# Kernel tuning notes

Measured on AMD Instinct MI355X. Metric: run time of the kernel, lower is better.

The kernel has to match this reference:

```python
import jax, jax.numpy as jnp
import numpy as np

# Layered-DAG regularization of the dynamic active_path graph.
H, N, BATCH, D, R = 6, 16, 32, 512, 64   # hop levels, nodes/level, batch, dim, low-rank
M = (H - 1) * N                           # nodes with weights (levels 1..H-1)
ETA_W = 0.015
LAM_C, LAM_R = 0.65, 0.35
THETA0 = 0.5
SPEC_MIN, SPEC_MAX = 0.3, 4.0
BETA1, BETA2, EPS = 0.9, 0.999, 1e-8
W_MAX = float(np.sqrt(D) * 2.0)
DW_CLIP = 5.0


def _spectral_norm(A1, B1):
    # largest singular value of W = A1 @ B1.T via power iteration using only low-rank products
    d = A1.shape[0]
    def body(_, u):
        w = A1 @ (B1.T @ (B1 @ (A1.T @ u)))  # (W W^T) u
        return w / (jnp.linalg.norm(w) + 1e-12)
    u0 = jnp.ones((d,), A1.dtype) / jnp.sqrt(jnp.asarray(d, A1.dtype))
    u = jax.lax.fori_loop(0, 20, body, u0)
    return jnp.linalg.norm(B1 @ (A1.T @ u))


def _update_node(A1, B1, mA, vA, mB, vB, Vin, T_local):
    # dual-signal (contrastive + retrograde) weight update, Adam step t=1, is_positive=True
    W = A1 @ B1.T                       # (D, D)
    Vw = Vin @ W.T                      # (BATCH, D) pre-activation (record.V_weighted)
    Vout = jnp.tanh(Vw)                 # record.V_out (tanh primitive)
    fprime = 1.0 - Vout ** 2            # primitive_derivative for tanh
    goodness = (Vout ** 2).sum(-1).mean()
    theta = THETA0 * ((Vin ** 2).sum(-1).mean() + 1e-9)   # goodness_scale_input=True
    delta = goodness - theta
    Vout_grad = (Vout * fprime * delta).mean(0)
    Vin_mean = Vin.mean(0)
    dW_c = jnp.outer(Vout_grad, Vin_mean)
    dW_r = jnp.outer(T_local.mean(0) * fprime.mean(0), Vin_mean)
    dW = LAM_C * dW_c + LAM_R * dW_r
    gnorm = jnp.linalg.norm(dW)
    dW = dW * jnp.where(gnorm > DW_CLIP, DW_CLIP / (gnorm + 1e-12), 1.0)
    gA = dW @ B1
    gB = dW.T @ A1
    mA_n = BETA1 * mA + (1 - BETA1) * gA
    vA_n = BETA2 * vA + (1 - BETA2) * gA ** 2
    A_new = A1 - ETA_W * (mA_n / (1 - BETA1)) / (jnp.sqrt(vA_n / (1 - BETA2)) + EPS)
    mB_n = BETA1 * mB + (1 - BETA1) * gB
    vB_n = BETA2 * vB + (1 - BETA2) * gB ** 2
    B_new = B1 - ETA_W * (mB_n / (1 - BETA1)) / (jnp.sqrt(vB_n / (1 - BETA2)) + EPS)
    return jnp.clip(A_new, -W_MAX, W_MAX), jnp.clip(B_new, -W_MAX, W_MAX)


def _forward(Y_hat, Y_star, V_edges, A, Bw, m_A, v_A, m_B, v_B):
    T_v = (Y_star - Y_hat) / jnp.sqrt(jnp.asarray(D, Y_hat.dtype))
    mse = jnp.mean((Y_star - Y_hat) ** 2)

    # proportional blame: per-edge mean-over-batch L2 norm of the contribution
    norms = jnp.linalg.norm(V_edges, axis=-1).mean(-1)           # (H-1, Ndst, Nsrc)
    w_blame = norms / (norms.sum(-1, keepdims=True) + 1e-9)

    spec = jax.vmap(jax.vmap(_spectral_norm))(A, Bw)             # (H-1, N)
    scale = jax.lax.stop_gradient(jnp.clip(spec, SPEC_MIN, SPEC_MAX))  # torch.tensor() detaches

    # retrograde flow in reverse topological (hop) order; output node = (level H-1, node 0)
    T_top = jnp.zeros((N, BATCH, D), Y_hat.dtype).at[0].set(T_v)

    def step(T_curr, xs):
        w_h, s_h = xs                                            # (Ndst,Nsrc), (Ndst,)
        tnorm = jnp.linalg.norm(T_curr, axis=-1).mean(-1)        # (Ndst,)
        edge_t = s_h[:, None] * w_h * tnorm[:, None]             # ||T_upstream|| per edge
        T_prev = jnp.einsum('j,ji,jbd->ibd', s_h, w_h, T_curr)   # blame-weighted scatter
        return T_prev, (T_prev, edge_t)

    _, (Ts, edge_t) = jax.lax.scan(step, T_top, (w_blame[::-1], scale[::-1]))
    T_all = jnp.concatenate([Ts[::-1], T_top[None]], axis=0)     # (H, N, BATCH, D), by level
    edge_tensions = edge_t[::-1]                                 # (H-1, Ndst, Nsrc)

    V_in = V_edges.sum(axis=2)                                   # inbox sum -> (H-1, N, BATCH, D)
    T_upd = T_all[1:]                                            # tensions at non-input nodes

    sh = (M, D, R)
    A_new, B_new = jax.vmap(_update_node)(
        A.reshape(sh), Bw.reshape(sh), m_A.reshape(sh), v_A.reshape(sh),
        m_B.reshape(sh), v_B.reshape(sh),
        V_in.reshape(M, BATCH, D), T_upd.reshape(M, BATCH, D))
    return (mse, edge_tensions,
            A_new.reshape(H - 1, N, D, R), B_new.reshape(H - 1, N, D, R), T_all)


def setup_inputs():
    key = jax.random.key(0)
    k = jax.random.split(key, 7)
    sd = 1.0 / np.sqrt(D)
    return {
        "Y_hat": jax.random.normal(k[0], (BATCH, D), jnp.float32),
        "Y_star": jax.random.normal(k[1], (BATCH, D), jnp.float32),
        "V_edges": jax.random.normal(k[2], (H - 1, N, N, BATCH, D), jnp.float32),
        "A": jax.random.normal(k[3], (H - 1, N, D, R), jnp.float32) * sd,
        "Bw": jax.random.normal(k[4], (H - 1, N, D, R), jnp.float32) * sd,
        "m_A": jnp.zeros((H - 1, N, D, R), jnp.float32),
        "v_A": jax.random.uniform(k[5], (H - 1, N, D, R), jnp.float32) * 1e-4,
        "m_B": jnp.zeros((H - 1, N, D, R), jnp.float32),
        "v_B": jax.random.uniform(k[6], (H - 1, N, D, R), jnp.float32) * 1e-4,
    }


def reference(Y_hat, Y_star, V_edges, A, Bw, m_A, v_A, m_B, v_B):
    return _forward(Y_hat, Y_star, V_edges, A, Bw, m_A, v_A, m_B, v_B)
```

## Files before the change

### kernel.cpp

```cpp
#include <hip/hip_runtime.h>
#include <math.h>

#define DEV static __device__ __forceinline__

constexpr int NB    = 16;
constexpr int BATCH = 32;
constexpr int DDIM  = 512;
constexpr int RK    = 64;
constexpr int LAY   = 5;
constexpr int MM    = 80;
constexpr int TLS   = NB * BATCH * DDIM;

constexpr float ETA_W   = 0.015f;
constexpr float LAM_C   = 0.65f, LAM_R = 0.35f;
constexpr float THETA0  = 0.5f;
constexpr float SPEC_MIN = 0.3f, SPEC_MAX = 4.0f;
constexpr float DW_CLIP = 5.0f;
constexpr float W_MAX   = 45.254833995939045f;
constexpr float RSQ_D   = 0.044194173824159216f;

constexpr int OUT_MSE  = 0;
constexpr int OUT_EDGE = 1;
constexpr int OUT_A    = 1281;
constexpr int OUT_B    = OUT_A + MM * DDIM * RK;
constexpr int OUT_T    = OUT_B + MM * DDIM * RK;

constexpr int SCR_GP   = 1284;
constexpr int SCR_VIN  = SCR_GP + 2621440;

constexpr int WS_NORMB  = 0;
constexpr int WS_TVN    = 40960;
constexpr int WS_COEF   = 40992;
constexpr int WS_C      = 43520;
constexpr int WS_SCALE  = 44800;
constexpr int WS_Y0P    = 44880;
constexpr int WS_VM     = 65360;
constexpr int WS_P      = 106320;
constexpr int WS_Q      = 111440;
constexpr int WS_GC     = 116560;

DEV float wave_reduce(float v) {
  #pragma unroll
  for (int o = 32; o > 0; o >>= 1) v += __shfl_down(v, o, 64);
  return v;
}

DEV float block_reduce_512(float v, float* sred) {
  v = wave_reduce(v);
  __syncthreads();
  if ((threadIdx.x & 63) == 0) sred[threadIdx.x >> 6] = v;
  __syncthreads();
  float s = 0.f;
  #pragma unroll
  for (int k = 0; k < 8; ++k) s += sred[k];
  return s;
}

DEV float bcast_lane(float v, int lane) {
  return __int_as_float(__builtin_amdgcn_readlane(__float_as_int(v), lane));
}

__global__ void kmse(const float* __restrict__ yh, const float* __restrict__ ys,
                     float* __restrict__ out) {
  __shared__ float sred[16];
  int t = threadIdx.x;
  float s = 0.f;
  for (int i = t; i < 4096; i += 1024) {
    float4 a = ((const float4*)yh)[i], b = ((const float4*)ys)[i];
    float d0 = b.x - a.x, d1 = b.y - a.y, d2 = b.z - a.z, d3 = b.w - a.w;
    s += d0*d0 + d1*d1 + d2*d2 + d3*d3;
  }
  s = wave_reduce(s);
  if ((t & 63) == 0) sred[t >> 6] = s;
  __syncthreads();
  if (t == 0) {
    float tot = 0.f;
    #pragma unroll
    for (int k = 0; k < 16; ++k) tot += sred[k];
    out[OUT_MSE] = tot * (1.f / 16384.f);
  }
}

__global__ void k_tvnorm(const float* __restrict__ yh, const float* __restrict__ ys,
                         float* __restrict__ ws) {
  __shared__ float sred[4];
  int b = blockIdx.x, t = threadIdx.x;
  float2 a = ((const float2*)(yh + (size_t)b * 512))[t];
  float2 c = ((const float2*)(ys + (size_t)b * 512))[t];
  float d0 = c.x - a.x, d1 = c.y - a.y;
  float s = d0*d0 + d1*d1;
  s = wave_reduce(s);
  if ((t & 63) == 0) sred[t >> 6] = s;
  __syncthreads();
  if (t == 0)
    ws[WS_TVN + b] = sqrtf(sred[0] + sred[1] + sred[2] + sred[3]) * RSQ_D;
}

__global__ void k_vin_norm(const float* __restrict__ V, float* __restrict__ out,
                           float* __restrict__ ws) {
  __shared__ float sbuf[16][256];
  int bid = blockIdx.x;
  int b = bid & 31, j = (bid >> 5) & 15, hh = bid >> 9;
  const float* base = V + (size_t)(((hh*16 + j)*16)*32 + b) * 512;
  int t = threadIdx.x;
  float ax = 0.f, ay = 0.f;
  #pragma unroll
  for (int i = 0; i < 16; ++i) {
    float2 vv = ((const float2*)(base + (size_t)i * 16384))[t];
    sbuf[i][t] = vv.x*vv.x + vv.y*vv.y;
    ax += vv.x; ay += vv.y;
  }
  float2 o; o.x = ax; o.y = ay;
  ((float2*)(out + SCR_VIN + (size_t)((hh*16 + j)*32 + b) * 512))[t] = o;
  __syncthreads();
  int w = t >> 6, lane = t & 63;
  #pragma unroll
  for (int k = 0; k < 4; ++k) {
    int i = w * 4 + k;
    float s = sbuf[i][lane] + sbuf[i][lane+64] + sbuf[i][lane+128] + sbuf[i][lane+192];
    s = wave_reduce(s);
    if (lane == 0)
      ws[WS_NORMB + (size_t)((hh*16 + j)*16 + i) * 32 + b] = sqrtf(s);
  }
}

__global__ void k_gram(const float* __restrict__ Aw, const float* __restrict__ Bww,
                       float* __restrict__ out, float* __restrict__ ws) {
  __shared__ float tile[128 * 64];
  __shared__ float y0s[4][64];
  int bid = blockIdx.x;
  int slice = bid & 3, side = (bid >> 2) & 1, m = bid >> 3;
  const float* src = (side ? Bww : Aw) + (size_t)m * 32768 + slice * 8192;
  int t = threadIdx.x;
  #pragma unroll
  for (int k = 0; k < 8; ++k)
    ((float4*)tile)[t + k * 256] = ((const float4*)src)[t + k * 256];
  __syncthreads();
  {
    int r = t & 63, q = t >> 6;
    float s = 0.f;
    #pragma unroll 8
    for (int dd = q * 32; dd < q * 32 + 32; ++dd) s += tile[dd * 64 + r];
    y0s[q][r] = s;
  }
  __syncthreads();
  if (side == 0 && t < 64)
    ws[WS_Y0P + (m * 4 + slice) * 64 + t] = y0s[0][t] + y0s[1][t] + y0s[2][t] + y0s[3][t];
  float acc[4][4];
  #pragma unroll
  for (int i = 0; i < 4; ++i)
    #pragma unroll
    for (int k = 0; k < 4; ++k) acc[i][k] = 0.f;
  int r1 = (t >> 4) * 4, r2 = (t & 15) * 4;
  #pragma unroll 4
  for (int dd = 0; dd < 128; ++dd) {
    float4 a1 = *(const float4*)&tile[dd * 64 + r1];
    float4 a2 = *(const float4*)&tile[dd * 64 + r2];
    float av[4] = {a1.x, a1.y, a1.z, a1.w};
    float bv[4] = {a2.x, a2.y, a2.z, a2.w};
    #pragma unroll
    for (int i = 0; i < 4; ++i)
      #pragma unroll
      for (int k = 0; k < 4; ++k) acc[i][k] += av[i] * bv[k];
  }
  float* outp = out + SCR_GP + (size_t)((m * 2 + side) * 4 + slice) * 4096;
  #pragma unroll
  for (int i = 0; i < 4; ++i) {
    float4 v; v.x = acc[i][0]; v.y = acc[i][1]; v.z = acc[i][2]; v.w = acc[i][3];
    *(float4*)&outp[(r1 + i) * 64 + r2] = v;
  }
}

__global__ __launch_bounds__(64, 1) void k_power(const float* __restrict__ out,
                                                 float* __restrict__ ws) {
  int m = blockIdx.x;
  int r = threadIdx.x;
  const float* gp = out + SCR_GP + (size_t)(m * 2 + 0) * 16384;
  const float* hp = out + SCR_GP + (size_t)(m * 2 + 1) * 16384;
  float Gc[64], Hc[64];
  #pragma unroll
  for (int c4 = 0; c4 < 16; ++c4) {
    const float* gb = gp + r * 64 + c4 * 4;
    float4 g0 = *(const float4*)(gb);
    float4 g1 = *(const float4*)(gb + 4096);
    float4 g2 = *(const float4*)(gb + 8192);
    float4 g3 = *(const float4*)(gb + 12288);
    Gc[c4*4+0] = g0.x+g1.x+g2.x+g3.x;
    Gc[c4*4+1] = g0.y+g1.y+g2.y+g3.y;
    Gc[c4*4+2] = g0.z+g1.z+g2.z+g3.z;
    Gc[c4*4+3] = g0.w+g1.w+g2.w+g3.w;
    const float* hb = hp + r * 64 + c4 * 4;
    float4 h0 = *(const float4*)(hb);
    float4 h1 = *(const float4*)(hb + 4096);
    float4 h2 = *(const float4*)(hb + 8192);
    float4 h3 = *(const float4*)(hb + 12288);
    Hc[c4*4+0] = h0.x+h1.x+h2.x+h3.x;
    Hc[c4*4+1] = h0.y+h1.y+h2.y+h3.y;
    Hc[c4*4+2] = h0.z+h1.z+h2.z+h3.z;
    Hc[c4*4+3] = h0.w+h1.w+h2.w+h3.w;
  }
  float y = (ws[WS_Y0P + (m*4+0)*64 + r] + ws[WS_Y0P + (m*4+1)*64 + r] +
             ws[WS_Y0P + (m*4+2)*64 + r] + ws[WS_Y0P + (m*4+3)*64 + r]) * RSQ_D;
  for (int it = 0; it < 20; ++it) {
    float z0 = 0.f, z1 = 0.f, z2 = 0.f, z3 = 0.f;
    #pragma unroll
    for (int c = 0; c < 16; ++c) {
      z0 = fmaf(Hc[c],      bcast_lane(y, c),      z0);
      z1 = fmaf(Hc[c + 16], bcast_lane(y, c + 16), z1);
      z2 = fmaf(Hc[c + 32], bcast_lane(y, c + 32), z2);
      z3 = fmaf(Hc[c + 48], bcast_lane(y, c + 48), z3);
    }
    float z = (z0 + z1) + (z2 + z3);
    float t0 = 0.f, t1 = 0.f, t2 = 0.f, t3 = 0.f;
    #pragma unroll
    for (int c = 0; c < 16; ++c) {
      t0 = fmaf(Gc[c],      bcast_lane(z, c),      t0);
      t1 = fmaf(Gc[c + 16], bcast_lane(z, c + 16), t1);
      t2 = fmaf(Gc[c + 32], bcast_lane(z, c + 32), t2);
      t3 = fmaf(Gc[c + 48], bcast_lane(z, c + 48), t3);
    }
    float tt = (t0 + t1) + (t2 + t3);
    float zt = z * tt;
    #pragma unroll
    for (int o = 32; o > 0; o >>= 1) zt += __shfl_xor(zt, o, 64);
    y = tt / (sqrtf(zt) + 1e-12f);
  }
  float z0 = 0.f, z1 = 0.f, z2 = 0.f, z3 = 0.f;
  #pragma unroll
  for (int c = 0; c < 16; ++c) {
    z0 = fmaf(Hc[c],      bcast_lane(y, c),      z0);
    z1 = fmaf(Hc[c + 16], bcast_lane(y, c + 16), z1);
    z2 = fmaf(Hc[c + 32], bcast_lane(y, c + 32), z2);
    z3 = fmaf(Hc[c + 48], bcast_lane(y, c + 48), z3);
  }
  float z = (z0 + z1) + (z2 + z3);
  float yz = y * z;
  #pragma unroll
  for (int o = 32; o > 0; o >>= 1) yz += __shfl_xor(yz, o, 64);
  if (r == 0)
    ws[WS_SCALE + m] = fminf(fmaxf(sqrtf(yz), SPEC_MIN), SPEC_MAX);
}

__global__ void k_coef(float* __restrict__ ws) {
  int hh = blockIdx.x, t = threadIdx.x;
  int j = t >> 4;
  const float* nb = ws + WS_NORMB + (size_t)(hh * 256 + t) * 32;
  float n = 0.f;
  #pragma unroll 8
  for (int b = 0; b < 32; ++b) n += nb[b];
  n *= (1.f / 32.f);
  float s = n;
  s += __shfl_xor(s, 1, 64);
  s += __shfl_xor(s, 2, 64);
  s += __shfl_xor(s, 4, 64);
  s += __shfl_xor(s, 8, 64);
  ws[WS_C + hh * 256 + t] = ws[WS_SCALE + hh * 16 + j] * n / (s + 1e-9f);
}

__global__ void k_chain(float* __restrict__ ws, float* __restrict__ out) {
  __shared__ float C[5 * 256];
  __shared__ float coef[6 * 16];
  int t = threadIdx.x;
  #pragma unroll
  for (int k = 0; k < 5; ++k) C[k * 256 + t] = ws[WS_C + k * 256 + t];
  if (t < 16) coef[5 * 16 + t] = (t == 0) ? 1.f : 0.f;
  __syncthreads();
  if (t < 16) {
    for (int h = 4; h >= 0; --h) {
      float s = 0.f;
      #pragma unroll
      for (int j = 0; j < 16; ++j) s += C[h * 256 + j * 16 + t] * coef[(h + 1) * 16 + j];
      coef[h * 16 + t] = s;
    }
  }
  __syncthreads();
  float tvs = 0.f;
  #pragma unroll
  for (int b = 0; b < 32; ++b) tvs += ws[WS_TVN + b];
  float tvmean = tvs * (1.f / 32.f);
  #pragma unroll
  for (int h = 0; h < 5; ++h)
    out[OUT_EDGE + h * 256 + t] = C[h * 256 + t] * coef[(h + 1) * 16 + (t >> 4)] * tvmean;
  if (t < 96) ws[WS_COEF + t] = coef[t];
}

__global__ void k_twrite(const float* __restrict__ yh, const float* __restrict__ ys,
                         const float* __restrict__ ws, float* __restrict__ out) {
  int gid = blockIdx.x * 256 + threadIdx.x;
  int li = gid >> 14;
  int bd = gid & 16383;
  float tv = (ys[bd] - yh[bd]) * RSQ_D;
  out[OUT_T + gid] = ws[WS_COEF + li] * tv;
}

constexpr int MTP = 516;
constexpr int YVP = 36;

__global__ __launch_bounds__(512) void k_node(const float* __restrict__ Aw,
    const float* __restrict__ Bww, const float* out_all, float* __restrict__ ws) {
  __shared__ float MT[64 * MTP];
  __shared__ float R2[4096];
  __shared__ float gcol[512];
  __shared__ float sred[8];
  int m = blockIdx.x;
  int t = threadIdx.x;
  const float* A1  = Aw  + (size_t)m * 32768;
  const float* B1  = Bww + (size_t)m * 32768;
  const float* Vin = out_all + SCR_VIN + (size_t)m * 16384;
  int hh = m >> 4, j = m & 15;
  const float* Tl = out_all + OUT_T + (size_t)(hh + 1) * TLS + (size_t)j * 16384;

  auto stageT = [&](const float* src) {
    #pragma unroll
    for (int ch = 0; ch < 16; ++ch) {
      int g = ch * 2048 + t * 4;
      int d = g >> 6, r = g & 63;
      float4 v = *(const float4*)(src + g);
      MT[(r+0)*MTP + d] = v.x;
      MT[(r+1)*MTP + d] = v.y;
      MT[(r+2)*MTP + d] = v.z;
      MT[(r+3)*MTP + d] = v.w;
    }
  };

  stageT(B1);
  __syncthreads();

  {
    int rl = t & 31, bq = t >> 5;
    int b0 = bq * 2;
    float a00 = 0.f, a01 = 0.f, a10 = 0.f, a11 = 0.f;
    const float4* vp0 = (const float4*)(Vin + (size_t)b0 * 512);
    const float4* vp1 = (const float4*)(Vin + (size_t)(b0 + 1) * 512);
    #pragma unroll 4
    for (int d4 = 0; d4 < 128; ++d4) {
      float4 m0 = *(const float4*)&MT[rl * MTP + d4 * 4];
      float4 m1 = *(const float4*)&MT[(rl + 32) * MTP + d4 * 4];
      float4 v0 = vp0[d4];
      float4 v1 = vp1[d4];
      a00 += m0.x*v0.x + m0.y*v0.y + m0.z*v0.z + m0.w*v0.w;
      a01 += m0.x*v1.x + m0.y*v1.y + m0.z*v1.z + m0.w*v1.w;
      a10 += m1.x*v0.x + m1.y*v0.y + m1.z*v0.z + m1.w*v0.w;
      a11 += m1.x*v1.x + m1.y*v1.y + m1.z*v1.z + m1.w*v1.w;
    }
    R2[rl * YVP + b0]            = a00;
    R2[rl * YVP + b0 + 1]        = a01;
    R2[(rl + 32) * YVP + b0]     = a10;
    R2[(rl + 32) * YVP + b0 + 1] = a11;
  }
  __syncthreads();
  if (t < 64) {
    float s = 0.f;
    #pragma unroll 8
    for (int b = 0; b < 32; ++b) s += R2[t * YVP + b];
    ws[WS_P + m * 64 + t] = s * (1.f / 32.f);
  }
  float tmean, ssin, ssvm;
  {
    int d = t;
    float sv = 0.f, sq = 0.f, st = 0.f;
    #pragma unroll 4
    for (int b = 0; b < 32; ++b) {
      float v = Vin[b * 512 + d];
      sv += v; sq += v * v;
      st += Tl[b * 512 + d];
    }
    float vmean = sv * (1.f / 32.f);
    tmean = st * (1.f / 32.f);
    ws[WS_VM + m * 512 + d] = vmean;
    ssin = block_reduce_512(sq, sred) * (1.f / 32.f);
    ssvm = block_reduce_512(vmean * vmean, sred);
  }
  __syncthreads();
  stageT(A1);
  __syncthreads();
  float gs = 0.f;
  float vga[4] = {0.f, 0.f, 0.f, 0.f}, fpa[4] = {0.f, 0.f, 0.f, 0.f};
  {
    int d4 = t >> 2, bg = t & 3;
    float acc[4][8];
    #pragma unroll
    for (int i = 0; i < 4; ++i)
      #pragma unroll
      for (int k = 0; k < 8; ++k) acc[i][k] = 0.f;
    #pragma unroll 2
    for (int rr = 0; rr < 64; ++rr) {
      float4 at = *(const float4*)&MT[rr * MTP + d4 * 4];
      float4 ya = *(const float4*)&R2[rr * YVP + bg * 8];
      float4 yb = *(const float4*)&R2[rr * YVP + bg * 8 + 4];
      float av[4] = {at.x, at.y, at.z, at.w};
      float yv[8] = {ya.x, ya.y, ya.z, ya.w, yb.x, yb.y, yb.z, yb.w};
      #pragma unroll
      for (int i = 0; i < 4; ++i)
        #pragma unroll
        for (int k = 0; k < 8; ++k) acc[i][k] += av[i] * yv[k];
    }
    #pragma unroll
    for (int i = 0; i < 4; ++i)
      #pragma unroll
      for (int k = 0; k < 8; ++k) {
        float vw = acc[i][k];
        float x = fminf(fmaxf(vw * 2.f, -40.f), 40.f);
        float e = __expf(x);
        float vo = (e - 1.f) / (e + 1.f);
        float fp = 1.f - vo * vo;
        gs += vo * vo;
        vga[i] += vo * fp;
        fpa[i] += fp;
      }
  }
  __syncthreads();
  {
    int d4 = t >> 2, bg = t & 3;
    #pragma unroll
    for (int i = 0; i < 4; ++i) {
      R2[bg * 512 + d4 * 4 + i] = vga[i];
      R2[2048 + bg * 512 + d4 * 4 + i] = fpa[i];
    }
  }
  float goodness = block_reduce_512(gs, sred) * (1.f / 32.f);
  float delta = goodness - THETA0 * (ssin + 1e-9f);
  {
    int d = t;
    float vg = R2[d] + R2[512 + d] + R2[1024 + d] + R2[1536 + d];
    float fp = R2[2048 + d] + R2[2048 + 512 + d] + R2[2048 + 1024 + d] + R2[2048 + 1536 + d];
    float g = LAM_C * delta * vg * (1.f / 32.f) + LAM_R * tmean * (fp * (1.f / 32.f));
    float gn2 = block_reduce_512(g * g, sred);
    float gnorm = sqrtf(gn2) * sqrtf(ssvm);
    float clipf = gnorm > DW_CLIP ? DW_CLIP / (gnorm + 1e-12f) : 1.f;
    float gcv = g * clipf;
    ws[WS_GC + m * 512 + d] = gcv;
    gcol[d] = gcv;
  }
  __syncthreads();
  {
    int r = t & 63, dq = t >> 6;
    float s = 0.f;
    #pragma unroll
    for (int k = 0; k < 16; ++k) {
      int d = dq * 64 + k * 4;
      float4 at = *(const float4*)&MT[r * MTP + d];
      float4 gv = *(const float4*)&gcol[d];
      s += at.x*gv.x + at.y*gv.y + at.z*gv.z + at.w*gv.w;
    }
    R2[dq * 64 + r] = s;
  }
  __syncthreads();
  if (t < 64) {
    float s = 0.f;
    #pragma unroll
    for (int p8 = 0; p8 < 8; ++p8) s += R2[p8 * 64 + t];
    ws[WS_Q + m * 64 + t] = s;
  }
}

__global__ void k_adam(const float* __restrict__ Aw, const float* __restrict__ Bww,
                       const float* __restrict__ mA, const float* __restrict__ vA,
                       const float* __restrict__ mB, const float* __restrict__ vB,
                       const float* __restrict__ ws, float* __restrict__ out) {
  int gid = blockIdx.x * 256 + threadIdx.x;
  const int half = MM * DDIM * RK;
  bool isB = gid >= half;
  int e = isB ? gid - half : gid;
  int m = e >> 15;
  int rem = e & 32767;
  int d = rem >> 6;
  int r = rem & 63;
  float g;
  const float *w0, *m0, *v0;
  int obase;
  if (!isB) {
    g = ws[WS_GC + m * 512 + d] * ws[WS_P + m * 64 + r];
    w0 = Aw; m0 = mA; v0 = vA; obase = OUT_A;
  } else {
    g = ws[WS_VM + m * 512 + d] * ws[WS_Q + m * 64 + r];
    w0 = Bww; m0 = mB; v0 = vB; obase = OUT_B;
  }
  float a  = w0[e], mm = m0[e], vv = v0[e];
  float mn = 0.9f * mm + 0.1f * g;
  float vn = 0.999f * vv + 0.001f * g * g;
  float u = a - ETA_W * (mn * 10.f) / (sqrtf(vn * 1000.f) + 1e-8f);
  u = fminf(fmaxf(u, -W_MAX), W_MAX);
  out[obase + e] = u;
}

extern "C" void kernel_launch(void* const* d_in, const int* in_sizes, int n_in,
                              void* d_out, int out_size, void* d_ws, size_t ws_size,
                              hipStream_t stream) {
  (void)in_sizes; (void)n_in; (void)out_size; (void)ws_size;
  const float* Yh = (const float*)d_in[0];
  const float* Ys = (const float*)d_in[1];
  const float* V  = (const float*)d_in[2];
  const float* Aw = (const float*)d_in[3];
  const float* Bw = (const float*)d_in[4];
  const float* mA = (const float*)d_in[5];
  const float* vA = (const float*)d_in[6];
  const float* mB = (const float*)d_in[7];
  const float* vB = (const float*)d_in[8];
  float* out = (float*)d_out;
  float* ws  = (float*)d_ws;

  kmse<<<1, 1024, 0, stream>>>(Yh, Ys, out);
  k_tvnorm<<<32, 256, 0, stream>>>(Yh, Ys, ws);
  k_vin_norm<<<2560, 256, 0, stream>>>(V, out, ws);
  k_gram<<<640, 256, 0, stream>>>(Aw, Bw, out, ws);
  k_power<<<80, 64, 0, stream>>>(out, ws);
  k_coef<<<5, 256, 0, stream>>>(ws);
  k_chain<<<1, 256, 0, stream>>>(ws, out);
  k_twrite<<<6144, 256, 0, stream>>>(Yh, Ys, ws, out);
  k_node<<<80, 512, 0, stream>>>(Aw, Bw, out, ws);
  k_adam<<<20480, 256, 0, stream>>>(Aw, Bw, mA, vA, mB, vB, ws, out);
}
```

Before: 126.8 us.

## Fuse kernels, merge gram and power iteration, compute T mean analytically

```diff
diff --git a/kernel.cpp b/kernel.cpp
--- a/kernel.cpp
+++ b/kernel.cpp
@@ -25,19 +25,17 @@
 constexpr int OUT_B    = OUT_A + MM * DDIM * RK;
 constexpr int OUT_T    = OUT_B + MM * DDIM * RK;
 
-constexpr int SCR_GP   = 1284;
-constexpr int SCR_VIN  = SCR_GP + 2621440;
+constexpr int SCR_VIN  = 2622724;
 
 constexpr int WS_NORMB  = 0;
 constexpr int WS_TVN    = 40960;
-constexpr int WS_COEF   = 40992;
-constexpr int WS_C      = 43520;
-constexpr int WS_SCALE  = 44800;
-constexpr int WS_Y0P    = 44880;
-constexpr int WS_VM     = 65360;
-constexpr int WS_P      = 106320;
-constexpr int WS_Q      = 111440;
-constexpr int WS_GC     = 116560;
+constexpr int WS_TVM    = 41000;
+constexpr int WS_COEF   = 41600;
+constexpr int WS_SCALE  = 41700;
+constexpr int WS_VM     = 42000;
+constexpr int WS_P      = 83000;
+constexpr int WS_Q      = 88200;
+constexpr int WS_GC     = 93400;
 
 DEV float wave_reduce(float v) {
   #pragma unroll
@@ -60,216 +58,220 @@
   return __int_as_float(__builtin_amdgcn_readlane(__float_as_int(v), lane));
 }
 
-__global__ void kmse(const float* __restrict__ yh, const float* __restrict__ ys,
-                     float* __restrict__ out) {
-  __shared__ float sred[16];
+__global__ __launch_bounds__(256) void k_stage1(const float* __restrict__ V,
+    const float* __restrict__ yh, const float* __restrict__ ys,
+    float* __restrict__ out, float* __restrict__ ws) {
+  __shared__ float sbuf[16][256];
+  int bid = blockIdx.x, t = threadIdx.x;
+  if (bid < 2560) {
+    int b = bid & 31, j = (bid >> 5) & 15, hh = bid >> 9;
+    const float* base = V + (size_t)(((hh*16 + j)*16)*32 + b) * 512;
+    float ax = 0.f, ay = 0.f;
+    #pragma unroll
+    for (int i = 0; i < 16; ++i) {
+      float2 vv = ((const float2*)(base + (size_t)i * 16384))[t];
+      sbuf[i][t] = vv.x*vv.x + vv.y*vv.y;
+      ax += vv.x; ay += vv.y;
+    }
+    float2 o; o.x = ax; o.y = ay;
+    ((float2*)(out + SCR_VIN + (size_t)((hh*16 + j)*32 + b) * 512))[t] = o;
+    __syncthreads();
+    int w = t >> 6, lane = t & 63;
+    #pragma unroll
+    for (int k = 0; k < 4; ++k) {
+      int i = w * 4 + k;
+      float s = sbuf[i][lane] + sbuf[i][lane+64] + sbuf[i][lane+128] + sbuf[i][lane+192];
+      s = wave_reduce(s);
+      if (lane == 0)
+        ws[WS_NORMB + (size_t)((hh*16 + j)*16 + i) * 32 + b] = sqrtf(s);
+    }
+  } else if (bid < 2592) {
+    int b = bid - 2560;
+    float2 a = ((const float2*)(yh + (size_t)b * 512))[t];
+    float2 c = ((const float2*)(ys + (size_t)b * 512))[t];
+    float d0 = c.x - a.x, d1 = c.y - a.y;
+    float s = d0*d0 + d1*d1;
+    s = wave_reduce(s);
+    if ((t & 63) == 0) sbuf[0][t >> 6] = s;
+    __syncthreads();
+    if (t == 0)
+      ws[WS_TVN + b] = sqrtf(sbuf[0][0]+sbuf[0][1]+sbuf[0][2]+sbuf[0][3]) * RSQ_D;
+  } else if (bid == 2592) {
+    float s = 0.f;
+    for (int i = t; i < 4096; i += 256) {
+      float4 a = ((const float4*)yh)[i], b = ((const float4*)ys)[i];
+      float d0 = b.x-a.x, d1 = b.y-a.y, d2 = b.z-a.z, d3 = b.w-a.w;
+      s += d0*d0 + d1*d1 + d2*d2 + d3*d3;
+    }
+    s = wave_reduce(s);
+    if ((t & 63) == 0) sbuf[0][t >> 6] = s;
+    __syncthreads();
+    if (t == 0)
+      out[OUT_MSE] = (sbuf[0][0]+sbuf[0][1]+sbuf[0][2]+sbuf[0][3]) * (1.f/16384.f);
+  } else {
+    float s0 = 0.f, s1 = 0.f;
+    #pragma unroll 4
+    for (int b = 0; b < 32; ++b) {
+      s0 += ys[b*512 + t]       - yh[b*512 + t];
+      s1 += ys[b*512 + t + 256] - yh[b*512 + t + 256];
+    }
+    ws[WS_TVM + t]       = s0 * (RSQ_D / 32.f);
+    ws[WS_TVM + t + 256] = s1 * (RSQ_D / 32.f);
+  }
+}
+
+__global__ __launch_bounds__(256) void k_gp(const float* __restrict__ Aw,
+                                            const float* __restrict__ Bww,
+                                            float* __restrict__ ws) {
+  __shared__ float tile[128 * 64];
+  __shared__ float GH[2][4096];
+  __shared__ float y0s[4][64];
+  int m = blockIdx.x;
   int t = threadIdx.x;
-  float s = 0.f;
-  for (int i = t; i < 4096; i += 1024) {
-    float4 a = ((const float4*)yh)[i], b = ((const float4*)ys)[i];
-    float d0 = b.x - a.x, d1 = b.y - a.y, d2 = b.z - a.z, d3 = b.w - a.w;
-    s += d0*d0 + d1*d1 + d2*d2 + d3*d3;
-  }
-  s = wave_reduce(s);
-  if ((t & 63) == 0) sred[t >> 6] = s;
-  __syncthreads();
-  if (t == 0) {
-    float tot = 0.f;
-    #pragma unroll
-    for (int k = 0; k < 16; ++k) tot += sred[k];
-    out[OUT_MSE] = tot * (1.f / 16384.f);
-  }
-}
-
-__global__ void k_tvnorm(const float* __restrict__ yh, const float* __restrict__ ys,
-                         float* __restrict__ ws) {
-  __shared__ float sred[4];
-  int b = blockIdx.x, t = threadIdx.x;
-  float2 a = ((const float2*)(yh + (size_t)b * 512))[t];
-  float2 c = ((const float2*)(ys + (size_t)b * 512))[t];
-  float d0 = c.x - a.x, d1 = c.y - a.y;
-  float s = d0*d0 + d1*d1;
-  s = wave_reduce(s);
-  if ((t & 63) == 0) sred[t >> 6] = s;
-  __syncthreads();
-  if (t == 0)
-    ws[WS_TVN + b] = sqrtf(sred[0] + sred[1] + sred[2] + sred[3]) * RSQ_D;
-}
-
-__global__ void k_vin_norm(const float* __restrict__ V, float* __restrict__ out,
-                           float* __restrict__ ws) {
-  __shared__ float sbuf[16][256];
-  int bid = blockIdx.x;
-  int b = bid & 31, j = (bid >> 5) & 15, hh = bid >> 9;
-  const float* base = V + (size_t)(((hh*16 + j)*16)*32 + b) * 512;
-  int t = threadIdx.x;
-  float ax = 0.f, ay = 0.f;
-  #pragma unroll
-  for (int i = 0; i < 16; ++i) {
-    float2 vv = ((const float2*)(base + (size_t)i * 16384))[t];
-    sbuf[i][t] = vv.x*vv.x + vv.y*vv.y;
-    ax += vv.x; ay += vv.y;
-  }
-  float2 o; o.x = ax; o.y = ay;
-  ((float2*)(out + SCR_VIN + (size_t)((hh*16 + j)*32 + b) * 512))[t] = o;
-  __syncthreads();
-  int w = t >> 6, lane = t & 63;
-  #pragma unroll
-  for (int k = 0; k < 4; ++k) {
-    int i = w * 4 + k;
-    float s = sbuf[i][lane] + sbuf[i][lane+64] + sbuf[i][lane+128] + sbuf[i][lane+192];
-    s = wave_reduce(s);
-    if (lane == 0)
-      ws[WS_NORMB + (size_t)((hh*16 + j)*16 + i) * 32 + b] = sqrtf(s);
-  }
-}
-
-__global__ void k_gram(const float* __restrict__ Aw, const float* __restrict__ Bww,
-                       float* __restrict__ out, float* __restrict__ ws) {
-  __shared__ float tile[128 * 64];
-  __shared__ float y0s[4][64];
-  int bid = blockIdx.x;
-  int slice = bid & 3, side = (bid >> 2) & 1, m = bid >> 3;
-  const float* src = (side ? Bww : Aw) + (size_t)m * 32768 + slice * 8192;
-  int t = threadIdx.x;
-  #pragma unroll
-  for (int k = 0; k < 8; ++k)
-    ((float4*)tile)[t + k * 256] = ((const float4*)src)[t + k * 256];
-  __syncthreads();
-  {
-    int r = t & 63, q = t >> 6;
-    float s = 0.f;
-    #pragma unroll 8
-    for (int dd = q * 32; dd < q * 32 + 32; ++dd) s += tile[dd * 64 + r];
-    y0s[q][r] = s;
-  }
-  __syncthreads();
-  if (side == 0 && t < 64)
-    ws[WS_Y0P + (m * 4 + slice) * 64 + t] = y0s[0][t] + y0s[1][t] + y0s[2][t] + y0s[3][t];
+  int r1 = (t >> 4) * 4, r2 = (t & 15) * 4;
+  const float* A1 = Aw  + (size_t)m * 32768;
+  const float* B1 = Bww + (size_t)m * 32768;
   float acc[4][4];
+  float y0acc = 0.f;
+
   #pragma unroll
   for (int i = 0; i < 4; ++i)
     #pragma unroll
     for (int k = 0; k < 4; ++k) acc[i][k] = 0.f;
-  int r1 = (t >> 4) * 4, r2 = (t & 15) * 4;
-  #pragma unroll 4
-  for (int dd = 0; dd < 128; ++dd) {
-    float4 a1 = *(const float4*)&tile[dd * 64 + r1];
-    float4 a2 = *(const float4*)&tile[dd * 64 + r2];
-    float av[4] = {a1.x, a1.y, a1.z, a1.w};
-    float bv[4] = {a2.x, a2.y, a2.z, a2.w};
-    #pragma unroll
-    for (int i = 0; i < 4; ++i)
-      #pragma unroll
-      for (int k = 0; k < 4; ++k) acc[i][k] += av[i] * bv[k];
-  }
-  float* outp = out + SCR_GP + (size_t)((m * 2 + side) * 4 + slice) * 4096;
-  #pragma unroll
-  for (int i = 0; i < 4; ++i) {
-    float4 v; v.x = acc[i][0]; v.y = acc[i][1]; v.z = acc[i][2]; v.w = acc[i][3];
-    *(float4*)&outp[(r1 + i) * 64 + r2] = v;
-  }
-}
-
-__global__ __launch_bounds__(64, 1) void k_power(const float* __restrict__ out,
-                                                 float* __restrict__ ws) {
-  int m = blockIdx.x;
-  int r = threadIdx.x;
-  const float* gp = out + SCR_GP + (size_t)(m * 2 + 0) * 16384;
-  const float* hp = out + SCR_GP + (size_t)(m * 2 + 1) * 16384;
-  float Gc[64], Hc[64];
-  #pragma unroll
-  for (int c4 = 0; c4 < 16; ++c4) {
-    const float* gb = gp + r * 64 + c4 * 4;
-    float4 g0 = *(const float4*)(gb);
-    float4 g1 = *(const float4*)(gb + 4096);
-    float4 g2 = *(const float4*)(gb + 8192);
-    float4 g3 = *(const float4*)(gb + 12288);
-    Gc[c4*4+0] = g0.x+g1.x+g2.x+g3.x;
-    Gc[c4*4+1] = g0.y+g1.y+g2.y+g3.y;
-    Gc[c4*4+2] = g0.z+g1.z+g2.z+g3.z;
-    Gc[c4*4+3] = g0.w+g1.w+g2.w+g3.w;
-    const float* hb = hp + r * 64 + c4 * 4;
-    float4 h0 = *(const float4*)(hb);
-    float4 h1 = *(const float4*)(hb + 4096);
-    float4 h2 = *(const float4*)(hb + 8192);
-    float4 h3 = *(const float4*)(hb + 12288);
-    Hc[c4*4+0] = h0.x+h1.x+h2.x+h3.x;
-    Hc[c4*4+1] = h0.y+h1.y+h2.y+h3.y;
-    Hc[c4*4+2] = h0.z+h1.z+h2.z+h3.z;
-    Hc[c4*4+3] = h0.w+h1.w+h2.w+h3.w;
-  }
-  float y = (ws[WS_Y0P + (m*4+0)*64 + r] + ws[WS_Y0P + (m*4+1)*64 + r] +
-             ws[WS_Y0P + (m*4+2)*64 + r] + ws[WS_Y0P + (m*4+3)*64 + r]) * RSQ_D;
-  for (int it = 0; it < 20; ++it) {
-    float z0 = 0.f, z1 = 0.f, z2 = 0.f, z3 = 0.f;
+  for (int slice = 0; slice < 4; ++slice) {
+    __syncthreads();
+    const float* src = A1 + slice * 8192;
+    #pragma unroll
+    for (int k = 0; k < 8; ++k)
+      ((float4*)tile)[t + k * 256] = ((const float4*)src)[t + k * 256];
+    __syncthreads();
+    {
+      int rr = t & 63, q = t >> 6;
+      float s = 0.f;
+      #pragma unroll 8
+      for (int dd = q*32; dd < q*32 + 32; ++dd) s += tile[dd*64 + rr];
+      y0s[q][rr] = s;
+    }
+    __syncthreads();
+    if (t < 64) y0acc += y0s[0][t] + y0s[1][t] + y0s[2][t] + y0s[3][t];
+    #pragma unroll 4
+    for (int dd = 0; dd < 128; ++dd) {
+      float4 a1 = *(const float4*)&tile[dd*64 + r1];
+      float4 a2 = *(const float4*)&tile[dd*64 + r2];
+      float av[4] = {a1.x, a1.y, a1.z, a1.w};
+      float bv[4] = {a2.x, a2.y, a2.z, a2.w};
+      #pragma unroll
+      for (int i = 0; i < 4; ++i)
+        #pragma unroll
+        for (int k = 0; k < 4; ++k) acc[i][k] += av[i] * bv[k];
+    }
+  }
+  #pragma unroll
+  for (int i = 0; i < 4; ++i)
+    #pragma unroll
+    for (int k = 0; k < 4; ++k) GH[0][(r1+i)*64 + r2+k] = acc[i][k];
+
+  #pragma unroll
+  for (int i = 0; i < 4; ++i)
+    #pragma unroll
+    for (int k = 0; k < 4; ++k) acc[i][k] = 0.f;
+  for (int slice = 0; slice < 4; ++slice) {
+    __syncthreads();
+    const float* src = B1 + slice * 8192;
+    #pragma unroll
+    for (int k = 0; k < 8; ++k)
+      ((float4*)tile)[t + k * 256] = ((const float4*)src)[t + k * 256];
+    __syncthreads();
+    #pragma unroll 4
+    for (int dd = 0; dd < 128; ++dd) {
+      float4 a1 = *(const float4*)&tile[dd*64 + r1];
+      float4 a2 = *(const float4*)&tile[dd*64 + r2];
+      float av[4] = {a1.x, a1.y, a1.z, a1.w};
+      float bv[4] = {a2.x, a2.y, a2.z, a2.w};
+      #pragma unroll
+      for (int i = 0; i < 4; ++i)
+        #pragma unroll
+        for (int k = 0; k < 4; ++k) acc[i][k] += av[i] * bv[k];
+    }
+  }
+  #pragma unroll
+  for (int i = 0; i < 4; ++i)
+    #pragma unroll
+    for (int k = 0; k < 4; ++k) GH[1][(r1+i)*64 + r2+k] = acc[i][k];
+  __syncthreads();
+
+  if (t < 64) {
+    int r = t;
+    float y = y0acc * RSQ_D;
+    for (int it = 0; it < 20; ++it) {
+      float z0=0.f, z1=0.f, z2=0.f, z3=0.f;
+      #pragma unroll
+      for (int c = 0; c < 16; ++c) {
+        z0 = fmaf(GH[1][ c      *64 + r], bcast_lane(y, c),      z0);
+        z1 = fmaf(GH[1][(c+16)*64 + r], bcast_lane(y, c+16),   z1);
+        z2 = fmaf(GH[1][(c+32)*64 + r], bcast_lane(y, c+32),   z2);
+        z3 = fmaf(GH[1][(c+48)*64 + r], bcast_lane(y, c+48),   z3);
+      }
+      float z = (z0+z1) + (z2+z3);
+      float t0=0.f, t1=0.f, t2=0.f, t3=0.f;
+      #pragma unroll
+      for (int c = 0; c < 16; ++c) {
+        t0 = fmaf(GH[0][ c      *64 + r], bcast_lane(z, c),      t0);
+        t1 = fmaf(GH[0][(c+16)*64 + r], bcast_lane(z, c+16),   t1);
+        t2 = fmaf(GH[0][(c+32)*64 + r], bcast_lane(z, c+32),   t2);
+        t3 = fmaf(GH[0][(c+48)*64 + r], bcast_lane(z, c+48),   t3);
+      }
+      float tt = (t0+t1) + (t2+t3);
+      float zt = z * tt;
+      #pragma unroll
+      for (int o = 32; o > 0; o >>= 1) zt += __shfl_xor(zt, o, 64);
+      y = tt / (sqrtf(zt) + 1e-12f);
+    }
+    float z0=0.f, z1=0.f, z2=0.f, z3=0.f;
     #pragma unroll
     for (int c = 0; c < 16; ++c) {
-      z0 = fmaf(Hc[c],      bcast_lane(y, c),      z0);
-      z1 = fmaf(Hc[c + 16], bcast_lane(y, c + 16), z1);
-      z2 = fmaf(Hc[c + 32], bcast_lane(y, c + 32), z2);
-      z3 = fmaf(Hc[c + 48], bcast_lane(y, c + 48), z3);
-    }
-    float z = (z0 + z1) + (z2 + z3);
-    float t0 = 0.f, t1 = 0.f, t2 = 0.f, t3 = 0.f;
-    #pragma unroll
-    for (int c = 0; c < 16; ++c) {
-      t0 = fmaf(Gc[c],      bcast_lane(z, c),      t0);
-      t1 = fmaf(Gc[c + 16], bcast_lane(z, c + 16), t1);
-      t2 = fmaf(Gc[c + 32], bcast_lane(z, c + 32), t2);
-      t3 = fmaf(Gc[c + 48], bcast_lane(z, c + 48), t3);
-    }
-    float tt = (t0 + t1) + (t2 + t3);
-    float zt = z * tt;
-    #pragma unroll
-    for (int o = 32; o > 0; o >>= 1) zt += __shfl_xor(zt, o, 64);
-    y = tt / (sqrtf(zt) + 1e-12f);
-  }
-  float z0 = 0.f, z1 = 0.f, z2 = 0.f, z3 = 0.f;
-  #pragma unroll
-  for (int c = 0; c < 16; ++c) {
-    z0 = fmaf(Hc[c],      bcast_lane(y, c),      z0);
-    z1 = fmaf(Hc[c + 16], bcast_lane(y, c + 16), z1);
-    z2 = fmaf(Hc[c + 32], bcast_lane(y, c + 32), z2);
-    z3 = fmaf(Hc[c + 48], bcast_lane(y, c + 48), z3);
-  }
-  float z = (z0 + z1) + (z2 + z3);
-  float yz = y * z;
-  #pragma unroll
-  for (int o = 32; o > 0; o >>= 1) yz += __shfl_xor(yz, o, 64);
-  if (r == 0)
-    ws[WS_SCALE + m] = fminf(fmaxf(sqrtf(yz), SPEC_MIN), SPEC_MAX);
-}
-
-__global__ void k_coef(float* __restrict__ ws) {
-  int hh = blockIdx.x, t = threadIdx.x;
-  int j = t >> 4;
-  const float* nb = ws + WS_NORMB + (size_t)(hh * 256 + t) * 32;
-  float n = 0.f;
-  #pragma unroll 8
-  for (int b = 0; b < 32; ++b) n += nb[b];
-  n *= (1.f / 32.f);
-  float s = n;
-  s += __shfl_xor(s, 1, 64);
-  s += __shfl_xor(s, 2, 64);
-  s += __shfl_xor(s, 4, 64);
-  s += __shfl_xor(s, 8, 64);
-  ws[WS_C + hh * 256 + t] = ws[WS_SCALE + hh * 16 + j] * n / (s + 1e-9f);
-}
-
-__global__ void k_chain(float* __restrict__ ws, float* __restrict__ out) {
+      z0 = fmaf(GH[1][ c      *64 + r], bcast_lane(y, c),      z0);
+      z1 = fmaf(GH[1][(c+16)*64 + r], bcast_lane(y, c+16),   z1);
+      z2 = fmaf(GH[1][(c+32)*64 + r], bcast_lane(y, c+32),   z2);
+      z3 = fmaf(GH[1][(c+48)*64 + r], bcast_lane(y, c+48),   z3);
+    }
+    float z = (z0+z1) + (z2+z3);
+    float yz = y * z;
+    #pragma unroll
+    for (int o = 32; o > 0; o >>= 1) yz += __shfl_xor(yz, o, 64);
+    if (r == 0)
+      ws[WS_SCALE + m] = fminf(fmaxf(sqrtf(yz), SPEC_MIN), SPEC_MAX);
+  }
+}
+
+__global__ __launch_bounds__(256) void k_cc(float* __restrict__ ws,
+                                            float* __restrict__ out) {
   __shared__ float C[5 * 256];
   __shared__ float coef[6 * 16];
   int t = threadIdx.x;
-  #pragma unroll
-  for (int k = 0; k < 5; ++k) C[k * 256 + t] = ws[WS_C + k * 256 + t];
+  int j = t >> 4;
+  #pragma unroll
+  for (int h = 0; h < 5; ++h) {
+    const float* nb = ws + WS_NORMB + (size_t)(h * 256 + t) * 32;
+    float n = 0.f;
+    #pragma unroll 8
+    for (int b = 0; b < 32; ++b) n += nb[b];
+    n *= (1.f / 32.f);
+    float s = n;
+    s += __shfl_xor(s, 1, 64);
+    s += __shfl_xor(s, 2, 64);
+    s += __shfl_xor(s, 4, 64);
+    s += __shfl_xor(s, 8, 64);
+    C[h * 256 + t] = ws[WS_SCALE + h * 16 + j] * n / (s + 1e-9f);
+  }
   if (t < 16) coef[5 * 16 + t] = (t == 0) ? 1.f : 0.f;
   __syncthreads();
   if (t < 16) {
     for (int h = 4; h >= 0; --h) {
       float s = 0.f;
       #pragma unroll
-      for (int j = 0; j < 16; ++j) s += C[h * 256 + j * 16 + t] * coef[(h + 1) * 16 + j];
+      for (int jj = 0; jj < 16; ++jj)
+        s += C[h * 256 + jj * 16 + t] * coef[(h + 1) * 16 + jj];
       coef[h * 16 + t] = s;
     }
   }
@@ -280,17 +282,8 @@
   float tvmean = tvs * (1.f / 32.f);
   #pragma unroll
   for (int h = 0; h < 5; ++h)
-    out[OUT_EDGE + h * 256 + t] = C[h * 256 + t] * coef[(h + 1) * 16 + (t >> 4)] * tvmean;
+    out[OUT_EDGE + h * 256 + t] = C[h * 256 + t] * coef[(h + 1) * 16 + j] * tvmean;
   if (t < 96) ws[WS_COEF + t] = coef[t];
-}
-
-__global__ void k_twrite(const float* __restrict__ yh, const float* __restrict__ ys,
-                         const float* __restrict__ ws, float* __restrict__ out) {
-  int gid = blockIdx.x * 256 + threadIdx.x;
-  int li = gid >> 14;
-  int bd = gid & 16383;
-  float tv = (ys[bd] - yh[bd]) * RSQ_D;
-  out[OUT_T + gid] = ws[WS_COEF + li] * tv;
 }
 
 constexpr int MTP = 516;
@@ -308,7 +301,7 @@
   const float* B1  = Bww + (size_t)m * 32768;
   const float* Vin = out_all + SCR_VIN + (size_t)m * 16384;
   int hh = m >> 4, j = m & 15;
-  const float* Tl = out_all + OUT_T + (size_t)(hh + 1) * TLS + (size_t)j * 16384;
+  float coefval = ws[WS_COEF + (hh + 1) * 16 + j];
 
   auto stageT = [&](const float* src) {
     #pragma unroll
@@ -358,15 +351,14 @@
   float tmean, ssin, ssvm;
   {
     int d = t;
-    float sv = 0.f, sq = 0.f, st = 0.f;
+    float sv = 0.f, sq = 0.f;
     #pragma unroll 4
     for (int b = 0; b < 32; ++b) {
       float v = Vin[b * 512 + d];
       sv += v; sq += v * v;
-      st += Tl[b * 512 + d];
     }
     float vmean = sv * (1.f / 32.f);
-    tmean = st * (1.f / 32.f);
+    tmean = coefval * ws[WS_TVM + d];
     ws[WS_VM + m * 512 + d] = vmean;
     ssin = block_reduce_512(sq, sred) * (1.f / 32.f);
     ssvm = block_reduce_512(vmean * vmean, sred);
@@ -454,34 +446,66 @@
   }
 }
 
-__global__ void k_adam(const float* __restrict__ Aw, const float* __restrict__ Bww,
-                       const float* __restrict__ mA, const float* __restrict__ vA,
-                       const float* __restrict__ mB, const float* __restrict__ vB,
-                       const float* __restrict__ ws, float* __restrict__ out) {
-  int gid = blockIdx.x * 256 + threadIdx.x;
-  const int half = MM * DDIM * RK;
-  bool isB = gid >= half;
-  int e = isB ? gid - half : gid;
+constexpr int TW_BLOCKS = 1536;
+constexpr int AD_HALF4  = 655360;
+
+__global__ __launch_bounds__(256) void k_final(const float* __restrict__ yh,
+    const float* __restrict__ ys,
+    const float* __restrict__ Aw, const float* __restrict__ Bww,
+    const float* __restrict__ mA, const float* __restrict__ vA,
+    const float* __restrict__ mB, const float* __restrict__ vB,
+    const float* __restrict__ ws, float* __restrict__ out) {
+  int bid = blockIdx.x, t = threadIdx.x;
+  if (bid < TW_BLOCKS) {
+    int g0 = (bid * 256 + t) * 4;
+    int li = g0 >> 14;
+    int bd = g0 & 16383;
+    float4 a = *(const float4*)(yh + bd);
+    float4 b = *(const float4*)(ys + bd);
+    float cf = ws[WS_COEF + li] * RSQ_D;
+    out[OUT_T + g0 + 0] = cf * (b.x - a.x);
+    out[OUT_T + g0 + 1] = cf * (b.y - a.y);
+    out[OUT_T + g0 + 2] = cf * (b.z - a.z);
+    out[OUT_T + g0 + 3] = cf * (b.w - a.w);
+    return;
+  }
+  int idx = (bid - TW_BLOCKS) * 256 + t;
+  bool isB = idx >= AD_HALF4;
+  int e = (isB ? idx - AD_HALF4 : idx) * 4;
   int m = e >> 15;
   int rem = e & 32767;
   int d = rem >> 6;
   int r = rem & 63;
-  float g;
+  float4 g4;
   const float *w0, *m0, *v0;
   int obase;
   if (!isB) {
-    g = ws[WS_GC + m * 512 + d] * ws[WS_P + m * 64 + r];
+    float gc = ws[WS_GC + m * 512 + d];
+    float4 p = *(const float4*)&ws[WS_P + m * 64 + r];
+    g4.x = gc * p.x; g4.y = gc * p.y; g4.z = gc * p.z; g4.w = gc * p.w;
     w0 = Aw; m0 = mA; v0 = vA; obase = OUT_A;
   } else {
-    g = ws[WS_VM + m * 512 + d] * ws[WS_Q + m * 64 + r];
+    float vm = ws[WS_VM + m * 512 + d];
+    float4 q = *(const float4*)&ws[WS_Q + m * 64 + r];
+    g4.x = vm * q.x; g4.y = vm * q.y; g4.z = vm * q.z; g4.w = vm * q.w;
     w0 = Bww; m0 = mB; v0 = vB; obase = OUT_B;
   }
-  float a  = w0[e], mm = m0[e], vv = v0[e];
-  float mn = 0.9f * mm + 0.1f * g;
-  float vn = 0.999f * vv + 0.001f * g * g;
-  float u = a - ETA_W * (mn * 10.f) / (sqrtf(vn * 1000.f) + 1e-8f);
-  u = fminf(fmaxf(u, -W_MAX), W_MAX);
-  out[obase + e] = u;
+  float4 a4 = *(const float4*)&w0[e];
+  float4 mm4 = *(const float4*)&m0[e];
+  float4 vv4 = *(const float4*)&v0[e];
+  float ga[4] = {g4.x, g4.y, g4.z, g4.w};
+  float aa[4] = {a4.x, a4.y, a4.z, a4.w};
+  float ma[4] = {mm4.x, mm4.y, mm4.z, mm4.w};
+  float va[4] = {vv4.x, vv4.y, vv4.z, vv4.w};
+  #pragma unroll
+  for (int i = 0; i < 4; ++i) {
+    float g = ga[i];
+    float mn = 0.9f * ma[i] + 0.1f * g;
+    float vn = 0.999f * va[i] + 0.001f * g * g;
+    float u = aa[i] - ETA_W * (mn * 10.f) / (sqrtf(vn * 1000.f) + 1e-8f);
+    u = fminf(fmaxf(u, -W_MAX), W_MAX);
+    out[obase + e + i] = u;
+  }
 }
 
 extern "C" void kernel_launch(void* const* d_in, const int* in_sizes, int n_in,
@@ -500,14 +524,10 @@
   float* out = (float*)d_out;
   float* ws  = (float*)d_ws;
 
-  kmse<<<1, 1024, 0, stream>>>(Yh, Ys, out);
-  k_tvnorm<<<32, 256, 0, stream>>>(Yh, Ys, ws);
-  k_vin_norm<<<2560, 256, 0, stream>>>(V, out, ws);
-  k_gram<<<640, 256, 0, stream>>>(Aw, Bw, out, ws);
-  k_power<<<80, 64, 0, stream>>>(out, ws);
-  k_coef<<<5, 256, 0, stream>>>(ws);
-  k_chain<<<1, 256, 0, stream>>>(ws, out);
-  k_twrite<<<6144, 256, 0, stream>>>(Yh, Ys, ws, out);
+  k_stage1<<<2594, 256, 0, stream>>>(V, Yh, Ys, out, ws);
+  k_gp<<<80, 256, 0, stream>>>(Aw, Bw, ws);
+  k_cc<<<1, 256, 0, stream>>>(ws, out);
   k_node<<<80, 512, 0, stream>>>(Aw, Bw, out, ws);
-  k_adam<<<20480, 256, 0, stream>>>(Aw, Bw, mA, vA, mB, vB, ws, out);
-}
+  k_final<<<TW_BLOCKS + 2 * (AD_HALF4 / 256), 256, 0, stream>>>(
+      Yh, Ys, Aw, Bw, mA, vA, mB, vB, ws, out);
+}
```

Result: slower. 133.6 us (+5.4%).
